# Kernel tuning notes

Measured on AMD Instinct MI355X. Metric: run time of the kernel, lower is better.

Reference implementation:

```python
import jax, jax.numpy as jnp
import numpy as np

NU, NI, E = 100000, 20000, 250000
H, HEADS, D, L = 128, 2, 64, 2


def setup_inputs() -> dict:
    key = jax.random.key(0)
    ks = jax.random.split(key, 12)
    s = 0.05  # glorot-ish init scale
    return {
        "x_user": jax.random.normal(ks[0], (NU, 64), jnp.float32),
        "x_item": jax.random.normal(ks[1], (NI, 128), jnp.float32),
        "Wp_user": jax.random.normal(ks[2], (64, H), jnp.float32) * s,
        "bp_user": jnp.zeros((H,), jnp.float32),
        "Wp_item": jax.random.normal(ks[3], (128, H), jnp.float32) * s,
        "bp_item": jnp.zeros((H,), jnp.float32),
        # stacked per [layer, relation] params; rel 0 = user->item, rel 1 = item->user
        "Wl": jax.random.normal(ks[4], (L, 2, H, H), jnp.float32) * s,  # source linear
        "bl": jnp.zeros((L, 2, H), jnp.float32),
        "Wr": jax.random.normal(ks[5], (L, 2, H, H), jnp.float32) * s,  # target linear
        "br": jnp.zeros((L, 2, H), jnp.float32),
        "att": jax.random.normal(ks[6], (L, 2, HEADS, D), jnp.float32) * s,
        "bias": jnp.zeros((L, 2, H), jnp.float32),
        "edge_src": jax.random.randint(ks[7], (E,), 0, NU, jnp.int32),  # user index per edge
        "edge_dst": jax.random.randint(ks[8], (E,), 0, NI, jnp.int32),  # item index per edge
    }


def _gatv2(x_src, x_dst, src, dst, wl, bl_, wr, br_, a, b_, n_dst):
    """One bipartite GATv2Conv (heads=HEADS, out=D, concat=True, eval mode)."""
    xl = (x_src @ wl + bl_).reshape(-1, HEADS, D)  # [Ns, h, d]
    xr = (x_dst @ wr + br_).reshape(-1, HEADS, D)  # [Nd, h, d]
    e = jax.nn.leaky_relu(xl[src] + xr[dst], 0.2)  # [E, h, d]
    logits = jnp.einsum('ehd,hd->eh', e, a)        # [E, h]
    # segment softmax over destination nodes (numerically stable)
    amax = jax.lax.stop_gradient(jax.ops.segment_max(logits, dst, num_segments=n_dst))
    p = jnp.exp(logits - amax[dst])
    denom = jax.ops.segment_sum(p, dst, num_segments=n_dst)
    alpha = p / (denom[dst] + 1e-16)               # PyG softmax epsilon
    msg = xl[src] * alpha[:, :, None]              # [E, h, d]
    out = jax.ops.segment_sum(msg, dst, num_segments=n_dst)  # [Nd, h, d]
    return out.reshape(n_dst, HEADS * D) + b_


def reference(x_user, x_item, Wp_user, bp_user, Wp_item, bp_item,
              Wl, bl, Wr, br, att, bias, edge_src, edge_dst):
    zu = x_user @ Wp_user + bp_user  # [NU, H]
    zi = x_item @ Wp_item + bp_item  # [NI, H]
    for l in range(L):
        zi_new = _gatv2(zu, zi, edge_src, edge_dst,
                        Wl[l, 0], bl[l, 0], Wr[l, 0], br[l, 0], att[l, 0], bias[l, 0], NI)
        zu_new = _gatv2(zi, zu, edge_dst, edge_src,
                        Wl[l, 1], bl[l, 1], Wr[l, 1], br[l, 1], att[l, 1], bias[l, 1], NU)
        zu, zi = zu_new, zi_new
        if l < L - 1:
            zu, zi = jax.nn.relu(zu), jax.nn.relu(zi)  # dropout is identity in eval
    return zu, zi
```

## Files before the change

### kernel.cpp

```cpp
#include <hip/hip_runtime.h>

#define HDIM 128

typedef __attribute__((ext_vector_type(8))) short short8;
typedef __attribute__((ext_vector_type(4))) float float4v;

__device__ __forceinline__ float b2f(unsigned short u){
  return __uint_as_float(((unsigned int)u) << 16);
}
__device__ __forceinline__ unsigned short f2b(float f){
  unsigned int x = __float_as_uint(f);
  x += 0x7fffu + ((x >> 16) & 1u);
  return (unsigned short)(x >> 16);
}

#if __has_builtin(__builtin_amdgcn_exp2f)
#define EXPX(x) __builtin_amdgcn_exp2f(x)
#define LOGSCALE 1.4426950408889634f
#else
#define EXPX(x) __expf(x)
#define LOGSCALE 1.f
#endif

__device__ __forceinline__ float dpp_red8(float x){
  x += __int_as_float(__builtin_amdgcn_update_dpp(0, __float_as_int(x), 0xB1, 0xF, 0xF, true));
  x += __int_as_float(__builtin_amdgcn_update_dpp(0, __float_as_int(x), 0x4E, 0xF, 0xF, true));
  x += __int_as_float(__builtin_amdgcn_update_dpp(0, __float_as_int(x), 0x141, 0xF, 0xF, true));
  return x;
}

__device__ __forceinline__ int sniff_block(const unsigned short* __restrict__ x){
  const int tid = threadIdx.x;
  int cnt = 0, tot = 0;
  for (int i = tid * 2; i < 4096; i += 512){
    float v = fabsf(b2f(x[i]));
    tot++;
    if (v > 1e-4f && v < 50.f) cnt++;
  }
  __shared__ int s_cnt[256], s_tot[256];
  s_cnt[tid] = cnt; s_tot[tid] = tot;
  __syncthreads();
  for (int o = 128; o > 0; o >>= 1){
    if (tid < o){ s_cnt[tid] += s_cnt[tid + o]; s_tot[tid] += s_tot[tid + o]; }
    __syncthreads();
  }
  __shared__ int res;
  if (tid == 0) res = (s_cnt[0] * 2 < s_tot[0]) ? 1 : 0;
  __syncthreads();
  return res;
}

#define P_WPU 0
#define P_WPI 8192
#define P_WL  24576
#define P_WR  90112
#define P_BL  155648
#define P_BR  156160
#define P_ATT 156672
#define P_BIA 157184
#define P_BPU 157696
#define P_BPI 157824
#define P_TOT 157952

struct CvtArgs { const void* src[10]; int len[10]; const unsigned short* xsniff; };

__global__ void cvt_all_kernel(CvtArgs args, unsigned short* __restrict__ P,
                               int* __restrict__ flag,
                               int* __restrict__ zero1, int nz1,
                               int* __restrict__ zero2, int nz2){
  const int f32 = sniff_block(args.xsniff);
  int t = blockIdx.x * 256 + threadIdx.x;
  if (t < nz1) zero1[t] = 0;
  if (t < nz2) zero2[t] = 0;
  if (t == 0) flag[0] = f32;
  if (t >= P_TOT) return;
  int local = t;
  int i = 0;
  while (local >= args.len[i]){ local -= args.len[i]; i++; }
  if (f32) P[t] = f2b(((const float*)args.src[i])[local]);
  else     P[t] = ((const unsigned short*)args.src[i])[local];
}

__global__ void prep_weights_kernel(const unsigned short* __restrict__ P,
                                    unsigned short* __restrict__ Wc)
{
  const int t = blockIdx.x * 256 + threadIdx.x;
  if (t >= 49664) return;
  const unsigned short* Wl = P + P_WL;
  const unsigned short* Wr = P + P_WR;
  const unsigned short* Bm[4] = { Wl, Wr + 16384, Wl + 16384, Wr };
  const unsigned short* Av[4] = { P + P_WPU, P + P_WPU, P + P_WPI, P + P_WPI };
  const unsigned short* bv[4] = { P + P_BPU, P + P_BPU, P + P_BPI, P + P_BPI };
  const unsigned short* bo[4] = { P + P_BL, P + P_BR + 128, P + P_BL + 128, P + P_BR };
  if (t < 49152){
    int job, base;
    if (t < 8192)       { job = 0; base = 0; }
    else if (t < 16384) { job = 1; base = 8192; }
    else if (t < 32768) { job = 2; base = 16384; }
    else                { job = 3; base = 32768; }
    const int local = t - base;
    const int k = local >> 7, n = local & 127;
    const unsigned short* A = Av[job] + (size_t)k * 128;
    const unsigned short* B = Bm[job];
    float s = 0.f;
    #pragma unroll 4
    for (int h = 0; h < 128; h++) s = fmaf(b2f(A[h]), b2f(B[h * 128 + n]), s);
    Wc[t] = f2b(s);
  } else {
    const int local = t - 49152;
    const int job = local >> 7, n = local & 127;
    const unsigned short* B = Bm[job];
    float s = b2f(bo[job][n]);
    for (int h = 0; h < 128; h++) s = fmaf(b2f(bv[job][h]), b2f(B[h * 128 + n]), s);
    Wc[t] = f2b(s);
  }
}

struct PermBiasArgs { const unsigned short* W0[4]; const unsigned short* W1[4];
                      int KS[4]; int base[4]; int n[4];
                      const unsigned short* blo[4]; const unsigned short* bhi[4]; };
__global__ void permute_bias_kernel(PermBiasArgs pa, unsigned short* __restrict__ dst,
                                    unsigned short* __restrict__ dstB){
  int t = blockIdx.x * 256 + threadIdx.x;
  if (t >= 114688){
    int u = t - 114688;
    if (u < 1024){
      int set = u >> 8, c = u & 255;
      dstB[u] = (c < 128) ? pa.blo[set][c] : pa.bhi[set][c - 128];
    }
    return;
  }
  int job = 0;
  while (job < 4 && t >= pa.base[job] + pa.n[job]) job++;
  if (job >= 4) return;
  int local = t - pa.base[job];
  int KS = pa.KS[job];
  int j = local & 7, rest = local >> 3;
  int l = rest & 63; rest >>= 6;
  int ks = rest % KS, tile = rest / KS;
  int k = ks * 32 + (l >> 4) * 8 + j;
  int c = tile * 16 + (l & 15);
  dst[t] = (c < 128) ? pa.W0[job][k * 128 + c] : pa.W1[job][k * 128 + (c - 128)];
}

template<int K>
__device__ __forceinline__ void linear_body(const void* __restrict__ Xv, int xstride,
                                            bool f32,
                                            const unsigned short* __restrict__ Bp,
                                            const unsigned short* __restrict__ bias,
                                            unsigned short* __restrict__ Y, int M, int bx,
                                            unsigned short* __restrict__ lds)
{
  constexpr int KS = K / 32;
  const int wave = threadIdx.x >> 6, lane = threadIdx.x & 63;
  const int quad = lane >> 4, l16 = lane & 15;
  const int row0 = bx * 64;

  float4v acc[4][4];
  const float4v z = {0.f, 0.f, 0.f, 0.f};
  #pragma unroll
  for (int i = 0; i < 4; i++)
    #pragma unroll
    for (int j = 0; j < 4; j++) acc[i][j] = z;

  for (int ks = 0; ks < KS; ks++){
    const int col = ks * 32 + quad * 8;
    short8 a[4];
    #pragma unroll
    for (int mt = 0; mt < 4; mt++){
      int r = row0 + mt * 16 + l16; if (r >= M) r = M - 1;
      if (f32){
        const float* p = (const float*)Xv + (size_t)r * xstride + col;
        float4 v0 = *(const float4*)p;
        float4 v1 = *(const float4*)(p + 4);
        short8 tmp;
        tmp[0] = (short)f2b(v0.x); tmp[1] = (short)f2b(v0.y);
        tmp[2] = (short)f2b(v0.z); tmp[3] = (short)f2b(v0.w);
        tmp[4] = (short)f2b(v1.x); tmp[5] = (short)f2b(v1.y);
        tmp[6] = (short)f2b(v1.z); tmp[7] = (short)f2b(v1.w);
        a[mt] = tmp;
      } else {
        a[mt] = *(const short8*)((const unsigned short*)Xv + (size_t)r * xstride + col);
      }
    }
    short8 b[4];
    #pragma unroll
    for (int ntl = 0; ntl < 4; ntl++){
      const int t = wave * 4 + ntl;
      b[ntl] = *(const short8*)(Bp + ((size_t)(t * KS + ks) * 64 + lane) * 8);
    }
    #pragma unroll
    for (int mt = 0; mt < 4; mt++)
      #pragma unroll
      for (int ntl = 0; ntl < 4; ntl++)
        acc[mt][ntl] = __builtin_amdgcn_mfma_f32_16x16x32_bf16(a[mt], b[ntl], acc[mt][ntl], 0, 0, 0);
  }

  #pragma unroll
  for (int mt = 0; mt < 4; mt++){
    #pragma unroll
    for (int ntl = 0; ntl < 4; ntl++){
      const int t = wave * 4 + ntl;
      const int colb = t * 16 + l16;
      const float bb = b2f(bias[colb]);
      #pragma unroll
      for (int r = 0; r < 4; r++){
        const int rl = mt * 16 + quad * 4 + r;
        lds[rl * 256 + colb] = f2b(acc[mt][ntl][r] + bb);
      }
    }
  }
  __syncthreads();
  const uint4* l4 = (const uint4*)lds;
  #pragma unroll
  for (int i = 0; i < 8; i++){
    const int idx = i * 256 + (int)threadIdx.x;
    const int row = idx >> 5;
    const int grow = row0 + row;
    if (grow < M)
      *((uint4*)(Y + (size_t)grow * 256) + (idx & 31)) = l4[idx];
  }
}

template<int KA, int KB>
__launch_bounds__(256)
__global__ void linear_both_kernel(const void* __restrict__ XA, int sA,
                                   const unsigned short* __restrict__ BpA,
                                   const unsigned short* __restrict__ biasA,
                                   unsigned short* __restrict__ YA, int MA, int gA,
                                   const void* __restrict__ XB, int sB,
                                   const unsigned short* __restrict__ BpB,
                                   const unsigned short* __restrict__ biasB,
                                   unsigned short* __restrict__ YB, int MB,
                                   const int* __restrict__ flag, int use_flag)
{
  __shared__ unsigned short lds[64 * 256];
  const bool f32 = use_flag && (*flag != 0);
  if ((int)blockIdx.x < gA) linear_body<KA>(XA, sA, f32, BpA, biasA, YA, MA, blockIdx.x, lds);
  else                      linear_body<KB>(XB, sB, f32, BpB, biasB, YB, MB, blockIdx.x - gA, lds);
}

__global__ void count_both_kernel(const int* __restrict__ esrc, const int* __restrict__ edst,
                                  int* __restrict__ degU, int* __restrict__ degI, int E){
  int t = blockIdx.x * 256 + threadIdx.x;
  if (t >= E) return;
  atomicAdd(&degI[edst[t]], 1);
  atomicAdd(&degU[esrc[t]], 1);
}

__global__ void scan_hist_par_kernel(const int* __restrict__ degI, const int* __restrict__ degU,
                                     int* __restrict__ rpI, int* __restrict__ rpU,
                                     int* __restrict__ blkI, int* __restrict__ blkU,
                                     int* __restrict__ histI, int* __restrict__ histU,
                                     int NI, int NU, int BI, int BU, int BI2, int BU2){
  const int tid = threadIdx.x;
  const int b = blockIdx.x;
  const int nscan = BI + BU;
  if (b < nscan){
    __shared__ int s[256];
    const int* deg; int* rowptr; int* blksum; int Nd; int bb;
    if (b < BI){ deg = degI; rowptr = rpI; blksum = blkI; Nd = NI; bb = b; }
    else       { deg = degU; rowptr = rpU; blksum = blkU; Nd = NU; bb = b - BI; }
    const int base = bb * 2048 + tid * 8;
    int v[8]; int tot = 0;
    #pragma unroll
    for (int j = 0; j < 8; j++){
      int idx = base + j;
      v[j] = (idx < Nd) ? deg[idx] : 0;
      tot += v[j];
    }
    s[tid] = tot;
    __syncthreads();
    for (int off = 1; off < 256; off <<= 1){
      int add = (tid >= off) ? s[tid - off] : 0;
      __syncthreads();
      s[tid] += add;
      __syncthreads();
    }
    int run = s[tid] - tot;
    #pragma unroll
    for (int j = 0; j < 8; j++){
      int idx = base + j;
      if (idx < Nd) rowptr[idx] = run;
      run += v[j];
    }
    if (tid == 255) blksum[bb] = s[255];
  } else {
    __shared__ int h2[64];
    if (tid < 64) h2[tid] = 0;
    __syncthreads();
    const int bb = b - nscan;
    const int* deg; int* gh; int base; int N;
    if (bb < BI2){ deg = degI; gh = histI; base = bb * 256; N = NI; }
    else         { deg = degU; gh = histU; base = (bb - BI2) * 256; N = NU; }
    const int n = base + tid;
    if (n < N) atomicAdd(&h2[min(deg[n], 63)], 1);
    __syncthreads();
    if (tid < 64 && h2[tid]) atomicAdd(&gh[tid], h2[tid]);
  }
}

__global__ void tops_kernel(int* __restrict__ blkI, int BI, int* __restrict__ blkU, int BU,
                            int* __restrict__ histI, int* __restrict__ histU){
  const int tid = threadIdx.x;
  const int lane = tid & 63;
  if (tid < 128){
    int* blk = (tid < 64) ? blkI : blkU;
    const int B = (tid < 64) ? BI : BU;
    int v = (lane < B) ? blk[lane] : 0;
    const int orig = v;
    #pragma unroll
    for (int off = 1; off < 64; off <<= 1){
      int u = __shfl_up(v, off, 64);
      if (lane >= off) v += u;
    }
    if (lane < B) blk[lane] = v - orig;
  } else {
    int* h = (tid < 192) ? histI : histU;
    int v = h[lane];
    int x = v;
    #pragma unroll
    for (int off = 1; off < 64; off <<= 1){
      int u = __shfl_down(x, off, 64);
      x += (lane + off < 64) ? u : 0;
    }
    h[lane] = x - v;
  }
}

__global__ void scan_add2_kernel(int* __restrict__ rpI, int* __restrict__ rpU,
                                 const int* __restrict__ blkI, const int* __restrict__ blkU,
                                 int* __restrict__ curI, int* __restrict__ curU,
                                 int NI, int NU, int BI, int E){
  const int b = blockIdx.x;
  int* rowptr; const int* blksum; int* curs; int Nd; int bb;
  if (b < BI){ rowptr = rpI; blksum = blkI; curs = curI; Nd = NI; bb = b; }
  else       { rowptr = rpU; blksum = blkU; curs = curU; Nd = NU; bb = b - BI; }
  const int base = bb * 2048 + threadIdx.x * 8;
  const int add = blksum[bb];
  #pragma unroll
  for (int j = 0; j < 8; j++){
    int idx = base + j;
    if (idx < Nd){ int v = rowptr[idx] + add; rowptr[idx] = v; curs[idx] = v; }
    else if (idx == Nd) rowptr[idx] = E;
  }
}

__global__ void scatter_all_kernel(const int* __restrict__ esrc, const int* __restrict__ edst,
                                   int* __restrict__ curI, int* __restrict__ curU,
                                   int* __restrict__ srcI, int* __restrict__ srcU,
                                   const int* __restrict__ rpI, const int* __restrict__ rpU,
                                   int* __restrict__ histI, int* __restrict__ histU,
                                   int* __restrict__ permI, int* __restrict__ permU,
                                   int NI, int NU, int E, int BI2, int BU2){
  const int tid = threadIdx.x;
  const int b = blockIdx.x;
  const int BP = BI2 + BU2;
  if (b < BP){
    __shared__ int h[64];
    __shared__ int cur[64];
    if (tid < 64) h[tid] = 0;
    __syncthreads();
    const int* rp; int* gh; int* perm; int base; int N;
    if (b < BI2){ rp = rpI; gh = histI; perm = permI; base = b * 256; N = NI; }
    else        { rp = rpU; gh = histU; perm = permU; base = (b - BI2) * 256; N = NU; }
    const int n = base + tid;
    int bk = -1;
    if (n < N){ int d = rp[n + 1] - rp[n]; bk = min(d, 63); atomicAdd(&h[bk], 1); }
    __syncthreads();
    if (tid < 64) cur[tid] = h[tid] ? atomicAdd(&gh[tid], h[tid]) : 0;
    __syncthreads();
    if (n < N){ int r = atomicAdd(&cur[bk], 1); perm[r] = n; }
  } else {
    int t = (b - BP) * 256 + tid;
    if (t < E){
      int d = edst[t];
      int pos = atomicAdd(&curI[d], 1);
      srcI[pos] = esrc[t];
    } else if (t < 2 * E){
      int tt = t - E;
      int d = esrc[tt];
      int pos = atomicAdd(&curU[d], 1);
      srcU[pos] = edst[tt];
    }
  }
}

struct GatRel {
  const unsigned short* zlrS;
  const unsigned short* zlrD;
  const int* rowptr;
  const int* srcArr;
  const int* perm;
  const unsigned short* att;
  const unsigned short* bias;
  void* out;
  unsigned long long elem_off;
  int Nd;
  int nw;
};

__launch_bounds__(256)
__global__ void fused_gat_sorted_kernel(GatRel A, GatRel B, int do_relu,
                                        const int* __restrict__ flag, int final_store)
{
  const int wave = threadIdx.x >> 6;
  const int lane = threadIdx.x & 63;
  const int ql = lane & 15;
  const int quad = lane >> 4;
  int gw = blockIdx.x * 4 + wave;
  GatRel R;
  if (gw < A.nw) R = A;
  else {
    gw -= A.nw;
    if (gw >= B.nw) return;
    R = B;
  }

  const int rank = gw * 4 + quad;
  const bool vnode = rank < R.Nd;
  int d = 0;
  if (vnode) d = R.perm[rank];
  int beg = 0, end = 0;
  if (vnode){ beg = R.rowptr[d]; end = R.rowptr[d + 1]; }
  int md = end - beg;
  md = max(md, __shfl_xor(md, 16, 64));
  md = max(md, __shfl_xor(md, 32, 64));

  const uint4* zlS4 = (const uint4*)R.zlrS;
  uint4 rv = ((const uint4*)R.zlrD)[(size_t)d * 32 + 16 + ql];
  float r[8], a[8];
  {
    const unsigned int* rp = (const unsigned int*)&rv;
    #pragma unroll
    for (int j = 0; j < 4; j++){
      r[2*j]   = __uint_as_float(rp[j] << 16);
      r[2*j+1] = __uint_as_float(rp[j] & 0xffff0000u);
    }
  }
  uint4 av = ((const uint4*)R.att)[ql];
  {
    const unsigned int* ap = (const unsigned int*)&av;
    #pragma unroll
    for (int j = 0; j < 4; j++){
      a[2*j]   = __uint_as_float(ap[j] << 16) * LOGSCALE;
      a[2*j+1] = __uint_as_float(ap[j] & 0xffff0000u) * LOGSCALE;
    }
  }

  float m = -1e30f, s = 0.f;
  float acc[8];
  #pragma unroll
  for (int j = 0; j < 8; j++) acc[j] = 0.f;

  if (md > 0){
    const int* sA = R.srcArr;
    int i1 = 0, i2 = 0;
    if (beg < end)     i1 = sA[beg];
    if (beg + 1 < end) i2 = sA[beg + 1];
    uint4 g0 = zlS4[(size_t)i1 * 32 + ql];

    for (int it = 0; it < md; it++){
      uint4 g1 = zlS4[(size_t)i2 * 32 + ql];
      int i3 = 0;
      { int ee = beg + it + 2; if (ee < end) i3 = sA[ee]; }
      const bool valid = (beg + it) < end;

      float x[8];
      const unsigned int* gp = (const unsigned int*)&g0;
      #pragma unroll
      for (int j = 0; j < 4; j++){
        x[2*j]   = __uint_as_float(gp[j] << 16);
        x[2*j+1] = __uint_as_float(gp[j] & 0xffff0000u);
      }
      float p = 0.f;
      #pragma unroll
      for (int j = 0; j < 8; j++){
        float t = x[j] + r[j];
        t = fmaxf(t, 0.2f * t);
        p = fmaf(a[j], t, p);
      }
      p = dpp_red8(p);
      const float pv = valid ? p : -1e30f;

      if (__builtin_expect(__any(pv > m + 8.f), 0)){
        const float mn = fmaxf(m, pv);
        const float scO = EXPX(m - mn);
        const float qv = valid ? EXPX(pv - mn) : 0.f;
        s = fmaf(s, scO, qv);
        #pragma unroll
        for (int j = 0; j < 8; j++) acc[j] = fmaf(acc[j], scO, x[j] * qv);
        m = mn;
      } else {
        const float qv = valid ? EXPX(pv - m) : 0.f;
        s += qv;
        #pragma unroll
        for (int j = 0; j < 8; j++) acc[j] = fmaf(x[j], qv, acc[j]);
      }
      g0 = g1; i2 = i3;
    }
  }

  const float inv = 1.f / (s + 1e-16f);
  uint4 bv = ((const uint4*)R.bias)[ql];
  float o[8];
  {
    const unsigned int* bp = (const unsigned int*)&bv;
    #pragma unroll
    for (int j = 0; j < 4; j++){
      o[2*j]   = fmaf(acc[2*j],   inv, __uint_as_float(bp[j] << 16));
      o[2*j+1] = fmaf(acc[2*j+1], inv, __uint_as_float(bp[j] & 0xffff0000u));
    }
  }
  if (do_relu){
    #pragma unroll
    for (int j = 0; j < 8; j++) o[j] = fmaxf(o[j], 0.f);
  }
  if (!vnode) return;
  const size_t eidx = (size_t)R.elem_off + (size_t)d * HDIM + 8 * ql;
  if (final_store && (*flag != 0)){
    float4 f0 = {o[0], o[1], o[2], o[3]};
    float4 f1 = {o[4], o[5], o[6], o[7]};
    float4* op = (float4*)R.out;
    op[eidx >> 2] = f0;
    op[(eidx >> 2) + 1] = f1;
  } else {
    uint4 w;
    unsigned int* wp = (unsigned int*)&w;
    #pragma unroll
    for (int j = 0; j < 4; j++)
      wp[j] = (unsigned int)f2b(o[2*j]) | ((unsigned int)f2b(o[2*j+1]) << 16);
    ((uint4*)R.out)[eidx >> 3] = w;
  }
}

extern "C" void kernel_launch(void* const* d_in, const int* in_sizes, int n_in,
                              void* d_out, int out_size, void* d_ws, size_t ws_size,
                              hipStream_t stream)
{
  const int* esrc = (const int*)d_in[12];
  const int* edst = (const int*)d_in[13];

  const int NU = in_sizes[0] / 64;
  const int NI = in_sizes[1] / 128;
  const int E  = in_sizes[12];
  const size_t fu = (size_t)NU * HDIM, fi = (size_t)NI * HDIM;

  char* w = (char*)d_ws;
  auto carve = [&](size_t bytes){ char* p = w; w += (bytes + 255) & ~(size_t)255; return p; };
  int* flag = (int*)carve(4);
  unsigned short* Wc = (unsigned short*)carve(49664 * 2);
  unsigned short* P  = (unsigned short*)carve((size_t)P_TOT * 2);
  unsigned short* Bp = (unsigned short*)carve(114688 * 2);
  unsigned short* Bc = (unsigned short*)carve(1024 * 2);
  int* rowptrI = (int*)carve(((size_t)NI + 1) * 4);
  int* rowptrU = (int*)carve(((size_t)NU + 1) * 4);
  int* curs    = (int*)carve(((size_t)NI + NU) * 4);
  int* cursI = curs;
  int* cursU = curs + NI;
  int* blkI = (int*)carve(64 * 4);
  int* blkU = (int*)carve(64 * 4);
  int* hists = (int*)carve(128 * 4);
  int* histI = hists;
  int* histU = hists + 64;
  int* permI = (int*)carve((size_t)NI * 4);
  int* permU = (int*)carve((size_t)NU * 4);
  int* srcI  = (int*)carve((size_t)E * 4);
  int* srcU  = (int*)carve((size_t)E * 4);
  unsigned short* zlrU = (unsigned short*)carve((size_t)NU * 256 * 2);
  unsigned short* zlrI = (unsigned short*)carve((size_t)NI * 256 * 2);
  (void)ws_size; (void)n_in; (void)out_size; (void)fi;

  unsigned short* stage_zu = (unsigned short*)d_out;
  unsigned short* stage_zi = (unsigned short*)d_out + fu;
  (void)stage_zi;

  CvtArgs ca;
  const int srcIdx[10] = {2, 4, 6, 8, 7, 9, 10, 11, 3, 5};
  const int lens[10] = {8192, 16384, 65536, 65536, 512, 512, 512, 512, 128, 128};
  for (int i = 0; i < 10; i++){ ca.src[i] = d_in[srcIdx[i]]; ca.len[i] = lens[i]; }
  ca.xsniff = (const unsigned short*)d_in[0];
  cvt_all_kernel<<<(P_TOT + 255) / 256, 256, 0, stream>>>(ca, P, flag,
                                                          curs, NI + NU, hists, 128);
  prep_weights_kernel<<<(49664 + 255) / 256, 256, 0, stream>>>(P, Wc);

  const unsigned short* cWlU0 = Wc;
  const unsigned short* cWrU1 = Wc + 8192;
  const unsigned short* cWlI1 = Wc + 16384;
  const unsigned short* cWrI0 = Wc + 32768;

  PermBiasArgs pa;
  pa.W0[0] = cWlU0;                 pa.W1[0] = cWrU1;                 pa.KS[0] = 2; pa.base[0] = 0;     pa.n[0] = 16384;
  pa.W0[1] = cWlI1;                 pa.W1[1] = cWrI0;                 pa.KS[1] = 4; pa.base[1] = 16384; pa.n[1] = 32768;
  pa.W0[2] = P + P_WL + 2 * 16384;  pa.W1[2] = P + P_WR + 3 * 16384;  pa.KS[2] = 4; pa.base[2] = 49152; pa.n[2] = 32768;
  pa.W0[3] = P + P_WL + 3 * 16384;  pa.W1[3] = P + P_WR + 2 * 16384;  pa.KS[3] = 4; pa.base[3] = 81920; pa.n[3] = 32768;
  pa.blo[0] = Wc + 49152;         pa.bhi[0] = Wc + 49152 + 128;
  pa.blo[1] = Wc + 49152 + 256;   pa.bhi[1] = Wc + 49152 + 384;
  pa.blo[2] = P + P_BL + 256;     pa.bhi[2] = P + P_BR + 384;
  pa.blo[3] = P + P_BL + 384;     pa.bhi[3] = P + P_BR + 256;
  permute_bias_kernel<<<(114688 + 1024 + 255) / 256, 256, 0, stream>>>(pa, Bp, Bc);
  unsigned short* BpU0 = Bp;
  unsigned short* BpI0 = Bp + 16384;
  unsigned short* BpU1 = Bp + 49152;
  unsigned short* BpI1 = Bp + 81920;

  const int BI = (NI + 2047) / 2048, BU = (NU + 2047) / 2048;
  const int BI2 = (NI + 255) / 256, BU2 = (NU + 255) / 256;
  count_both_kernel<<<(E + 255) / 256, 256, 0, stream>>>(esrc, edst, cursU, cursI, E);
  scan_hist_par_kernel<<<BI + BU + BI2 + BU2, 256, 0, stream>>>(
      cursI, cursU, rowptrI, rowptrU, blkI, blkU, histI, histU,
      NI, NU, BI, BU, BI2, BU2);
  tops_kernel<<<1, 256, 0, stream>>>(blkI, BI, blkU, BU, histI, histU);
  scan_add2_kernel<<<BI + BU, 256, 0, stream>>>(rowptrI, rowptrU, blkI, blkU, cursI, cursU, NI, NU, BI, E);
  scatter_all_kernel<<<BI2 + BU2 + (2 * E + 255) / 256, 256, 0, stream>>>(
      esrc, edst, cursI, cursU, srcI, srcU, rowptrI, rowptrU,
      histI, histU, permI, permU, NI, NU, E, BI2, BU2);

  const int gMU = (NU + 63) / 64, gMI = (NI + 63) / 64;
  const int nwA = (NI + 3) / 4, nwB = (NU + 3) / 4;
  const int gGat = (nwA + nwB + 3) / 4;

  for (int l = 0; l < 2; l++){
    if (l == 0){
      linear_both_kernel<64, 128><<<gMU + gMI, 256, 0, stream>>>(
          d_in[0], 64, BpU0, Bc, zlrU, NU, gMU,
          d_in[1], 128, BpI0, Bc + 256, zlrI, NI, flag, 1);
    } else {
      linear_both_kernel<128, 128><<<gMU + gMI, 256, 0, stream>>>(
          stage_zu, 128, BpU1, Bc + 512, zlrU, NU, gMU,
          stage_zi, 128, BpI1, Bc + 768, zlrI, NI, flag, 0);
    }
    const int relu = (l == 0);
    const int final_store = (l == 1);

    GatRel A, B;
    A.zlrS = zlrU; A.zlrD = zlrI; A.rowptr = rowptrI; A.srcArr = srcI; A.perm = permI;
    A.att  = P + P_ATT + (l * 2 + 0) * HDIM;
    A.bias = P + P_BIA + (l * 2 + 0) * HDIM;
    A.out = final_store ? d_out : (void*)stage_zu; A.elem_off = fu; A.Nd = NI; A.nw = nwA;
    B.zlrS = zlrI; B.zlrD = zlrU; B.rowptr = rowptrU; B.srcArr = srcU; B.perm = permU;
    B.att  = P + P_ATT + (l * 2 + 1) * HDIM;
    B.bias = P + P_BIA + (l * 2 + 1) * HDIM;
    B.out = final_store ? d_out : (void*)stage_zu; B.elem_off = 0; B.Nd = NU; B.nw = nwB;

    fused_gat_sorted_kernel<<<gGat, 256, 0, stream>>>(A, B, relu, flag, final_store);
  }
}
```

Measured before the change: 317.1 us.

## Stage linear input tile in LDS and write outputs directly from MFMA accumulators

The linear kernel now loads the 64xK input tile cooperatively into padded LDS with coalesced vector loads, converting fp32 to bf16 once. Previously each wave re-read the same rows from global memory. The MFMA A-fragments are then read from LDS. The LDS-staged coalesced output store is replaced by direct scattered 2-byte global stores from the accumulators, which may coalesce worse. The LDS footprint shrinks, which may raise occupancy.

```diff
diff --git a/kernel.cpp b/kernel.cpp
--- a/kernel.cpp
+++ b/kernel.cpp
@@ -152,9 +152,33 @@
                                             unsigned short* __restrict__ lds)
 {
   constexpr int KS = K / 32;
+  constexpr int LK = K + 8;
+  constexpr int ROUNDS = (64 * K) / 2048;
   const int wave = threadIdx.x >> 6, lane = threadIdx.x & 63;
   const int quad = lane >> 4, l16 = lane & 15;
   const int row0 = bx * 64;
+
+  #pragma unroll
+  for (int rd = 0; rd < ROUNDS; rd++){
+    const int e = rd * 2048 + (int)threadIdx.x * 8;
+    const int rr = e / K, cc = e % K;
+    int grow = row0 + rr; if (grow >= M) grow = M - 1;
+    unsigned short* dst = lds + rr * LK + cc;
+    if (f32){
+      const float* p = (const float*)Xv + (size_t)grow * xstride + cc;
+      float4 v0 = *(const float4*)p;
+      float4 v1 = *(const float4*)(p + 4);
+      short8 tmp;
+      tmp[0] = (short)f2b(v0.x); tmp[1] = (short)f2b(v0.y);
+      tmp[2] = (short)f2b(v0.z); tmp[3] = (short)f2b(v0.w);
+      tmp[4] = (short)f2b(v1.x); tmp[5] = (short)f2b(v1.y);
+      tmp[6] = (short)f2b(v1.z); tmp[7] = (short)f2b(v1.w);
+      *(short8*)dst = tmp;
+    } else {
+      *(short8*)dst = *(const short8*)((const unsigned short*)Xv + (size_t)grow * xstride + cc);
+    }
+  }
+  __syncthreads();
 
   float4v acc[4][4];
   const float4v z = {0.f, 0.f, 0.f, 0.f};
@@ -163,26 +187,13 @@
     #pragma unroll
     for (int j = 0; j < 4; j++) acc[i][j] = z;
 
+  #pragma unroll
   for (int ks = 0; ks < KS; ks++){
     const int col = ks * 32 + quad * 8;
     short8 a[4];
     #pragma unroll
-    for (int mt = 0; mt < 4; mt++){
-      int r = row0 + mt * 16 + l16; if (r >= M) r = M - 1;
-      if (f32){
-        const float* p = (const float*)Xv + (size_t)r * xstride + col;
-        float4 v0 = *(const float4*)p;
-        float4 v1 = *(const float4*)(p + 4);
-        short8 tmp;
-        tmp[0] = (short)f2b(v0.x); tmp[1] = (short)f2b(v0.y);
-        tmp[2] = (short)f2b(v0.z); tmp[3] = (short)f2b(v0.w);
-        tmp[4] = (short)f2b(v1.x); tmp[5] = (short)f2b(v1.y);
-        tmp[6] = (short)f2b(v1.z); tmp[7] = (short)f2b(v1.w);
-        a[mt] = tmp;
-      } else {
-        a[mt] = *(const short8*)((const unsigned short*)Xv + (size_t)r * xstride + col);
-      }
-    }
+    for (int mt = 0; mt < 4; mt++)
+      a[mt] = *(const short8*)(lds + (mt * 16 + l16) * LK + col);
     short8 b[4];
     #pragma unroll
     for (int ntl = 0; ntl < 4; ntl++){
@@ -205,20 +216,10 @@
       const float bb = b2f(bias[colb]);
       #pragma unroll
       for (int r = 0; r < 4; r++){
-        const int rl = mt * 16 + quad * 4 + r;
-        lds[rl * 256 + colb] = f2b(acc[mt][ntl][r] + bb);
+        const int row = row0 + mt * 16 + quad * 4 + r;
+        if (row < M) Y[(size_t)row * 256 + colb] = f2b(acc[mt][ntl][r] + bb);
       }
     }
-  }
-  __syncthreads();
-  const uint4* l4 = (const uint4*)lds;
-  #pragma unroll
-  for (int i = 0; i < 8; i++){
-    const int idx = i * 256 + (int)threadIdx.x;
-    const int row = idx >> 5;
-    const int grow = row0 + row;
-    if (grow < M)
-      *((uint4*)(Y + (size_t)grow * 256) + (idx & 31)) = l4[idx];
   }
 }
 
@@ -234,7 +235,7 @@
                                    unsigned short* __restrict__ YB, int MB,
                                    const int* __restrict__ flag, int use_flag)
 {
-  __shared__ unsigned short lds[64 * 256];
+  __shared__ unsigned short lds[64 * 136];
   const bool f32 = use_flag && (*flag != 0);
   if ((int)blockIdx.x < gA) linear_body<KA>(XA, sA, f32, BpA, biasA, YA, MA, blockIdx.x, lds);
   else                      linear_body<KB>(XB, sB, f32, BpB, biasB, YB, MB, blockIdx.x - gA, lds);
```

Measured after the change: 301.2 us. 1.05x faster.
